# Kernel tuning notes

Measured on AMD Instinct MI355X. Metric: run time of the kernel, lower is better.

Reference implementation:

```python
import jax, jax.numpy as jnp
import numpy as np

E, D_MODEL, D_FF = 8, 1024, 4096
B, S = 4, 2048


def setup_inputs() -> dict:
    key = jax.random.key(0)
    ks = jax.random.split(key, 7)
    scale_in = 1.0 / np.sqrt(D_MODEL)
    scale_ff = 1.0 / np.sqrt(D_FF)
    return {
        "x": jax.random.normal(ks[0], (B, S, D_MODEL), dtype=jnp.float32),
        "w1": jax.random.normal(ks[1], (E, D_MODEL, D_FF), dtype=jnp.float32) * scale_in,
        "b1": jax.random.normal(ks[2], (E, D_FF), dtype=jnp.float32) * 0.01,
        "w2": jax.random.normal(ks[3], (E, D_FF, D_MODEL), dtype=jnp.float32) * scale_ff,
        "b2": jax.random.normal(ks[4], (E, D_MODEL), dtype=jnp.float32) * 0.01,
        "gate_w": jax.random.normal(ks[5], (D_MODEL, E), dtype=jnp.float32) * scale_in,
        "gate_b": jax.random.normal(ks[6], (E,), dtype=jnp.float32) * 0.01,
    }


def reference(x, w1, b1, w2, b2, gate_w, gate_b):
    # Gating: softmax then top-1 (argmax of probs == argmax of logits)
    gate_logits = x @ gate_w + gate_b                      # [B,S,E]
    gate_probs = jax.nn.softmax(gate_logits, axis=-1)
    top1 = jnp.argmax(gate_probs, axis=-1)                 # [B,S] int
    mask = jax.nn.one_hot(top1, E, dtype=x.dtype)          # [B,S,E]

    # Dense compute of every expert on every token (faithful to source)
    h = jax.nn.relu(jnp.einsum('bsd,edf->ebsf', x, w1) + b1[:, None, None, :])  # [E,B,S,F]
    y = jnp.einsum('ebsf,efd->ebsd', h, w2) + b2[:, None, None, :]              # [E,B,S,D]

    # Top-1 mask-and-sum combine (note: no gate-prob scaling in the original)
    out = jnp.einsum('ebsd,bse->bsd', y, mask)             # [B,S,D]
    return out
```

## Files before the change

### kernel.cpp

```cpp
#include <hip/hip_runtime.h>
#include <stdint.h>

#define DM 1024
#define DF 4096
#define NE 8
#define NTOK 8192
#define MT256 40

typedef __attribute__((ext_vector_type(8))) short short8;
typedef __attribute__((ext_vector_type(8))) unsigned short ushort8v;
typedef __attribute__((ext_vector_type(4))) float floatx4;

__device__ inline unsigned short f2bf(float f) {
    union { float f; unsigned u; } v; v.f = f;
    unsigned u = v.u;
    u += 0x7fffu + ((u >> 16) & 1u);
    return (unsigned short)(u >> 16);
}

#define GLDS(g, l) __builtin_amdgcn_global_load_lds( \
    (const __attribute__((address_space(1))) void*)(g), \
    (__attribute__((address_space(3))) void*)(l), 16, 0, 0)

#define VMW(N)  asm volatile("s_waitcnt vmcnt(" #N ")" ::: "memory")
#define SCHED0  __builtin_amdgcn_sched_barrier(0)
#define BAR     __builtin_amdgcn_s_barrier()

__global__ __launch_bounds__(256) void gate_transpose(
    const float* __restrict__ x, const float* __restrict__ gw, const float* __restrict__ gb,
    int* __restrict__ top1, unsigned short* __restrict__ xb,
    const float* __restrict__ w1, unsigned short* __restrict__ w1t,
    const float* __restrict__ w2, unsigned short* __restrict__ w2t) {
    constexpr int GATE_BLKS = NTOK / 4;
    constexpr int NT1 = NE * (DM / 64) * (DF / 64);
    __shared__ float tile[64][65];
    int bid = blockIdx.x;
    int tid = threadIdx.x;

    if (bid < GATE_BLKS) {
        int wave = tid >> 6, lane = tid & 63;
        int t = bid * 4 + wave;
        const float* xr = x + (size_t)t * DM;
        unsigned short* xbr = xb + (size_t)t * DM;
        double acc[NE];
#pragma unroll
        for (int e = 0; e < NE; ++e) acc[e] = 0.0;
        for (int j = 0; j < DM / 64; ++j) {
            int d = j * 64 + lane;
            float xf = xr[d];
            xbr[d] = f2bf(xf);
            double xv = (double)xf;
            const float* g = gw + (size_t)d * NE;
#pragma unroll
            for (int e = 0; e < NE; ++e) acc[e] = fma(xv, (double)g[e], acc[e]);
        }
#pragma unroll
        for (int e = 0; e < NE; ++e) {
            for (int off = 32; off > 0; off >>= 1)
                acc[e] += __shfl_down(acc[e], off, 64);
        }
        if (lane == 0) {
            int best = 0;
            double bv = acc[0] + (double)gb[0];
            for (int e = 1; e < NE; ++e) {
                double v = acc[e] + (double)gb[e];
                if (v > bv) { bv = v; best = e; }
            }
            top1[t] = best;
        }
        return;
    }

    bid -= GATE_BLKS;
    const float* src; unsigned short* dst; int R, C;
    if (bid < NT1) { src = w1; dst = w1t; R = DM; C = DF; }
    else           { bid -= NT1; src = w2; dst = w2t; R = DF; C = DM; }
    int tilesR = R >> 6, tilesC = C >> 6;
    int e = bid / (tilesR * tilesC);
    int rem = bid % (tilesR * tilesC);
    int tr = rem / tilesC, tc = rem % tilesC;
    const float* s = src + (size_t)e * R * C + (size_t)(tr * 64) * C + tc * 64;
    unsigned short* d = dst + (size_t)e * R * C + (size_t)(tc * 64) * R + tr * 64;
#pragma unroll
    for (int i = 0; i < 4; ++i) {
        int idx = i * 256 + tid;
        int r = idx >> 4, c4 = (idx & 15) * 4;
        float4 v = *(const float4*)(s + (size_t)r * C + c4);
        tile[r][c4 + 0] = v.x; tile[r][c4 + 1] = v.y;
        tile[r][c4 + 2] = v.z; tile[r][c4 + 3] = v.w;
    }
    __syncthreads();
#pragma unroll
    for (int i = 0; i < 2; ++i) {
        int idx = i * 256 + tid;
        int c = idx >> 3, r8 = (idx & 7) * 8;
        ushort8v o;
#pragma unroll
        for (int j = 0; j < 8; ++j) o[j] = f2bf(tile[r8 + j][c]);
        *(ushort8v*)(d + (size_t)c * R + r8) = o;
    }
}

__global__ __launch_bounds__(1024) void sort_kernel(const int* __restrict__ top1,
                                                    int* __restrict__ ctrl,
                                                    int* __restrict__ perm) {
    __shared__ int cnt[NE];
    __shared__ int cur[NE];
    int tid = threadIdx.x, lane = tid & 63;
    if (tid < NE) cnt[tid] = 0;
    __syncthreads();
    int ev[8];
#pragma unroll
    for (int j = 0; j < 8; ++j) ev[j] = top1[j * 1024 + tid];
#pragma unroll
    for (int e = 0; e < NE; ++e) {
        int c = 0;
#pragma unroll
        for (int j = 0; j < 8; ++j) {
            unsigned long long m = __ballot(ev[j] == e);
            c += __popcll(m);
        }
        if (lane == 0) atomicAdd(&cnt[e], c);
    }
    __syncthreads();
    if (tid == 0) {
        int s = 0, t256 = 0;
        for (int e = 0; e < NE; ++e) {
            int c = cnt[e];
            cur[e] = s;
            for (int m = 0; m * 256 < c; ++m) {
                ctrl[32 + 3 * t256] = e;
                ctrl[33 + 3 * t256] = s + m * 256;
                int rr = c - m * 256;
                ctrl[34 + 3 * t256] = rr < 256 ? rr : 256;
                ++t256;
            }
            s += c;
        }
        ctrl[25] = t256;
    }
    __syncthreads();
#pragma unroll
    for (int j = 0; j < 8; ++j) {
        int e = ev[j];
#pragma unroll
        for (int ex = 0; ex < NE; ++ex) {
            unsigned long long m = __ballot(e == ex);
            if (m == 0ull) continue;
            int leader = __ffsll((long long)m) - 1;
            int base = 0;
            if (lane == leader) base = atomicAdd(&cur[ex], __popcll(m));
            base = __shfl(base, leader, 64);
            if (e == ex) {
                int pos = __popcll(m & ((1ull << lane) - 1ull));
                perm[base + pos] = j * 1024 + tid;
            }
        }
    }
}

#define F_SLAB(u, SU, STG, W) do { \
    if (STG) { \
        int kk_ = ((SU) + 3) * 32; \
        GLDS(ap0 + kk_, &As[((u) + 3) & 3][(size_t)tid * 8]); \
        GLDS(ap1 + kk_, &As[((u) + 3) & 3][(size_t)(512 + tid) * 8]); \
        GLDS(bp0 + kk_, &Bs[((u) + 3) & 3][(size_t)tid * 8]); \
        GLDS(bp1 + kk_, &Bs[((u) + 3) & 3][(size_t)(512 + tid) * 8]); \
    } \
    short8 bf[4], af[4], ag[4]; \
    _Pragma("unroll") \
    for (int n_ = 0; n_ < 4; ++n_) bf[n_] = *(const short8*)&Bs[u][boff[n_]]; \
    _Pragma("unroll") \
    for (int m_ = 0; m_ < 4; ++m_) af[m_] = *(const short8*)&As[u][aoff[m_]]; \
    _Pragma("unroll") \
    for (int m_ = 0; m_ < 4; ++m_) ag[m_] = *(const short8*)&As[u][aoff[4 + m_]]; \
    __builtin_amdgcn_s_setprio(1); \
    _Pragma("unroll") \
    for (int m_ = 0; m_ < 4; ++m_) \
        _Pragma("unroll") \
        for (int n_ = 0; n_ < 4; ++n_) \
            acc[m_][n_] = __builtin_amdgcn_mfma_f32_16x16x32_bf16(af[m_], bf[n_], acc[m_][n_], 0, 0, 0); \
    _Pragma("unroll") \
    for (int m_ = 0; m_ < 4; ++m_) \
        _Pragma("unroll") \
        for (int n_ = 0; n_ < 4; ++n_) \
            acc[4 + m_][n_] = __builtin_amdgcn_mfma_f32_16x16x32_bf16(ag[m_], bf[n_], acc[4 + m_][n_], 0, 0, 0); \
    __builtin_amdgcn_s_setprio(0); \
    W; SCHED0; BAR; \
} while (0)

template<bool FFN1>
__global__ __launch_bounds__(512, 2) void ffn_gemm(
    const unsigned short* __restrict__ A,
    const unsigned short* __restrict__ Bt,
    const float* __restrict__ bias,
    const int* __restrict__ ctrl,
    const int* __restrict__ perm,
    unsigned short* __restrict__ Hout,
    float* __restrict__ Yout) {
    constexpr int K = FFN1 ? DM : DF;
    constexpr int N = FFN1 ? DF : DM;
    constexpr int NT = N / 256;
    constexpr int NKI = K / 32;
    constexpr int SLABSZ = 256 * 32;
    constexpr int G = 8;

    int nwg = gridDim.x;
    int bo = blockIdx.x;
    int q = nwg >> 3, r = nwg & 7;
    int xcd = bo & 7, lid = bo >> 3;
    int b = (xcd < r ? xcd * (q + 1) : r * (q + 1) + (xcd - r) * q) + lid;

    int grp = b / (G * NT);
    int ii = b % (G * NT);
    int nt = ii / G;
    int til = grp * G + (ii % G);
    if (til >= ctrl[25]) return;
    int e       = ctrl[32 + 3 * til];
    int rowbase = ctrl[33 + 3 * til];
    int rows    = ctrl[34 + 3 * til];

    __shared__ __align__(16) unsigned short As[4][SLABSZ];
    __shared__ __align__(16) unsigned short Bs[4][SLABSZ];

    int tid = threadIdx.x, lane = tid & 63, wave = tid >> 6;
    int wm = (wave >> 2) * 128;
    int wn = (wave & 3) * 64;

    int rA0 = tid >> 2, rA1 = 128 + (tid >> 2);
    int kofs = ((tid & 3) ^ ((tid >> 3) & 3)) * 8;
    int c0 = rowbase + (rA0 < rows ? rA0 : rows - 1);
    int c1 = rowbase + (rA1 < rows ? rA1 : rows - 1);
    const unsigned short* ap0;
    const unsigned short* ap1;
    if (FFN1) {
        ap0 = A + (size_t)perm[c0] * K + kofs;
        ap1 = A + (size_t)perm[c1] * K + kofs;
    } else {
        ap0 = A + (size_t)c0 * K + kofs;
        ap1 = A + (size_t)c1 * K + kofs;
    }
    const unsigned short* bb  = Bt + (size_t)e * N * K + (size_t)(nt * 256) * K + kofs;
    const unsigned short* bp0 = bb + (size_t)rA0 * K;
    const unsigned short* bp1 = bb + (size_t)rA1 * K;

    int aoff[8], boff[4];
#pragma unroll
    for (int m = 0; m < 8; ++m) {
        int R = wm + m * 16 + (lane & 15);
        aoff[m] = R * 32 + (((lane >> 4) ^ ((R >> 1) & 3)) * 8);
    }
#pragma unroll
    for (int n = 0; n < 4; ++n) {
        int R = wn + n * 16 + (lane & 15);
        boff[n] = R * 32 + (((lane >> 4) ^ ((R >> 1) & 3)) * 8);
    }

    floatx4 acc[8][4];
#pragma unroll
    for (int i = 0; i < 8; ++i)
#pragma unroll
        for (int j = 0; j < 4; ++j) acc[i][j] = floatx4{0.f, 0.f, 0.f, 0.f};

#pragma unroll
    for (int s = 0; s < 3; ++s) {
        GLDS(ap0 + s * 32, &As[s][(size_t)tid * 8]);
        GLDS(ap1 + s * 32, &As[s][(size_t)(512 + tid) * 8]);
        GLDS(bp0 + s * 32, &Bs[s][(size_t)tid * 8]);
        GLDS(bp1 + s * 32, &Bs[s][(size_t)(512 + tid) * 8]);
    }
    VMW(8); SCHED0; BAR;

#pragma unroll 1
    for (int s = 0; s < NKI - 4; s += 4) {
        F_SLAB(0, s + 0, 1, VMW(8));
        F_SLAB(1, s + 1, 1, VMW(8));
        F_SLAB(2, s + 2, 1, VMW(8));
        F_SLAB(3, s + 3, 1, VMW(8));
    }
    F_SLAB(0, NKI - 4, 1, VMW(8));
    F_SLAB(1, NKI - 3, 0, VMW(4));
    F_SLAB(2, NKI - 2, 0, VMW(0));
    F_SLAB(3, NKI - 1, 0, (void)0);

    int col0 = nt * 256 + wn + (lane & 15);
    int rowq = (lane >> 4) * 4;
    float bv[4];
#pragma unroll
    for (int n = 0; n < 4; ++n) bv[n] = bias[e * N + col0 + n * 16];

#pragma unroll
    for (int m = 0; m < 8; ++m) {
#pragma unroll
        for (int r2 = 0; r2 < 4; ++r2) {
            int lr = wm + m * 16 + rowq + r2;
            if (lr < rows) {
                if (FFN1) {
                    unsigned short* hr = Hout + (size_t)(rowbase + lr) * DF + col0;
#pragma unroll
                    for (int n = 0; n < 4; ++n) {
                        float v = acc[m][n][r2] + bv[n];
                        v = v > 0.f ? v : 0.f;
                        hr[n * 16] = f2bf(v);
                    }
                } else {
                    float* yr = Yout + (size_t)perm[rowbase + lr] * DM + col0;
#pragma unroll
                    for (int n = 0; n < 4; ++n)
                        yr[n * 16] = acc[m][n][r2] + bv[n];
                }
            }
        }
    }
}
#undef F_SLAB

extern "C" void kernel_launch(void* const* d_in, const int* in_sizes, int n_in,
                              void* d_out, int out_size, void* d_ws, size_t ws_size,
                              hipStream_t stream) {
    const float* x  = (const float*)d_in[0];
    const float* w1 = (const float*)d_in[1];
    const float* b1 = (const float*)d_in[2];
    const float* w2 = (const float*)d_in[3];
    const float* b2 = (const float*)d_in[4];
    const float* gw = (const float*)d_in[5];
    const float* gb = (const float*)d_in[6];
    float* out = (float*)d_out;

    char* ws = (char*)d_ws;
    int* ctrl = (int*)ws;
    int* top1 = (int*)(ws + 2048);
    int* perm = (int*)(ws + 2048 + 32768);
    size_t o = 67584;
    unsigned short* xb  = (unsigned short*)(ws + o);        o += (size_t)NTOK * DM * 2;
    unsigned short* w1t = (unsigned short*)(ws + o);        o += (size_t)NE * DM * DF * 2;
    unsigned short* w2t = (unsigned short*)(ws + o);        o += (size_t)NE * DM * DF * 2;
    unsigned short* H   = (unsigned short*)(ws + o);

    gate_transpose<<<NTOK / 4 + 2 * NE * (DM / 64) * (DF / 64), 256, 0, stream>>>(
        x, gw, gb, top1, xb, w1, w1t, w2, w2t);
    sort_kernel<<<1, 1024, 0, stream>>>(top1, ctrl, perm);
    ffn_gemm<true ><<<MT256 * (DF / 256), 512, 0, stream>>>(xb, w1t, b1, ctrl, perm, H, nullptr);
    ffn_gemm<false><<<MT256 * (DM / 256), 512, 0, stream>>>(H, w2t, b2, ctrl, perm, nullptr, out);
}
```

Baseline: 562.0 us.

## Drop LDS tile from weight transpose and wait for all LDS reads before MFMAs

The weight transpose kernel no longer stages a 64x65 float tile in shared memory. Each thread reads 16 strided rows of one column directly from global memory, converts them to bf16 and writes 16 contiguous outputs. This removes LDS traffic and a barrier but makes the global reads column-strided. In the GEMM slab, all A and B fragment loads are now issued together, followed by an explicit lgkmcnt(0) wait and a scheduling barrier before the MFMA block. That gives up the overlap of LDS reads with the first group of MFMAs.

```diff
diff --git a/kernel.cpp b/kernel.cpp
--- a/kernel.cpp
+++ b/kernel.cpp
@@ -23,6 +23,7 @@
     (__attribute__((address_space(3))) void*)(l), 16, 0, 0)
 
 #define VMW(N)  asm volatile("s_waitcnt vmcnt(" #N ")" ::: "memory")
+#define LGKM0   asm volatile("s_waitcnt lgkmcnt(0)" ::: "memory")
 #define SCHED0  __builtin_amdgcn_sched_barrier(0)
 #define BAR     __builtin_amdgcn_s_barrier()
 
@@ -33,7 +34,6 @@
     const float* __restrict__ w2, unsigned short* __restrict__ w2t) {
     constexpr int GATE_BLKS = NTOK / 4;
     constexpr int NT1 = NE * (DM / 64) * (DF / 64);
-    __shared__ float tile[64][65];
     int bid = blockIdx.x;
     int tid = threadIdx.x;
 
@@ -81,24 +81,17 @@
     int tr = rem / tilesC, tc = rem % tilesC;
     const float* s = src + (size_t)e * R * C + (size_t)(tr * 64) * C + tc * 64;
     unsigned short* d = dst + (size_t)e * R * C + (size_t)(tc * 64) * R + tr * 64;
-#pragma unroll
-    for (int i = 0; i < 4; ++i) {
-        int idx = i * 256 + tid;
-        int r = idx >> 4, c4 = (idx & 15) * 4;
-        float4 v = *(const float4*)(s + (size_t)r * C + c4);
-        tile[r][c4 + 0] = v.x; tile[r][c4 + 1] = v.y;
-        tile[r][c4 + 2] = v.z; tile[r][c4 + 3] = v.w;
-    }
-    __syncthreads();
-#pragma unroll
-    for (int i = 0; i < 2; ++i) {
-        int idx = i * 256 + tid;
-        int c = idx >> 3, r8 = (idx & 7) * 8;
-        ushort8v o;
-#pragma unroll
-        for (int j = 0; j < 8; ++j) o[j] = f2bf(tile[r8 + j][c]);
-        *(ushort8v*)(d + (size_t)c * R + r8) = o;
-    }
+    int nl = tid & 63, kc = tid >> 6;
+    float v[16];
+#pragma unroll
+    for (int j = 0; j < 16; ++j)
+        v[j] = s[(size_t)(kc * 16 + j) * C + nl];
+    ushort8v oa, ob;
+#pragma unroll
+    for (int j = 0; j < 8; ++j) { oa[j] = f2bf(v[j]); ob[j] = f2bf(v[8 + j]); }
+    unsigned short* dp = d + (size_t)nl * R + kc * 16;
+    *(ushort8v*)(dp) = oa;
+    *(ushort8v*)(dp + 8) = ob;
 }
 
 __global__ __launch_bounds__(1024) void sort_kernel(const int* __restrict__ top1,
@@ -167,24 +160,18 @@
         GLDS(bp0 + kk_, &Bs[((u) + 3) & 3][(size_t)tid * 8]); \
         GLDS(bp1 + kk_, &Bs[((u) + 3) & 3][(size_t)(512 + tid) * 8]); \
     } \
-    short8 bf[4], af[4], ag[4]; \
+    short8 af[8], bf[4]; \
+    _Pragma("unroll") \
+    for (int m_ = 0; m_ < 8; ++m_) af[m_] = *(const short8*)&As[u][aoff[m_]]; \
     _Pragma("unroll") \
     for (int n_ = 0; n_ < 4; ++n_) bf[n_] = *(const short8*)&Bs[u][boff[n_]]; \
-    _Pragma("unroll") \
-    for (int m_ = 0; m_ < 4; ++m_) af[m_] = *(const short8*)&As[u][aoff[m_]]; \
-    _Pragma("unroll") \
-    for (int m_ = 0; m_ < 4; ++m_) ag[m_] = *(const short8*)&As[u][aoff[4 + m_]]; \
+    LGKM0; SCHED0; \
     __builtin_amdgcn_s_setprio(1); \
     _Pragma("unroll") \
-    for (int m_ = 0; m_ < 4; ++m_) \
+    for (int m_ = 0; m_ < 8; ++m_) \
         _Pragma("unroll") \
         for (int n_ = 0; n_ < 4; ++n_) \
             acc[m_][n_] = __builtin_amdgcn_mfma_f32_16x16x32_bf16(af[m_], bf[n_], acc[m_][n_], 0, 0, 0); \
-    _Pragma("unroll") \
-    for (int m_ = 0; m_ < 4; ++m_) \
-        _Pragma("unroll") \
-        for (int n_ = 0; n_ < 4; ++n_) \
-            acc[4 + m_][n_] = __builtin_amdgcn_mfma_f32_16x16x32_bf16(ag[m_], bf[n_], acc[4 + m_][n_], 0, 0, 0); \
     __builtin_amdgcn_s_setprio(0); \
     W; SCHED0; BAR; \
 } while (0)
```

New measurement: 590.4 us. 1.05x slower.
